# Kernel tuning notes

Measured on AMD Instinct MI355X. Metric: run time of the kernel, lower is better.

Reference implementation:

```python
import jax, jax.numpy as jnp
import numpy as np

B = 1024      # total windows (batch*windows_per_image)
W = 7         # window_size
T = W * W     # tokens per window = 49
C = 256       # scaled_emb_dim = emb_dim * 2**level
H = 8         # heads
D = C // H    # head_dim = 32
NUM_POS = 2 * W - 1


def _relative_pos():
    coords = np.arange(W)
    coords = np.stack(np.meshgrid(coords, coords, indexing='ij')).reshape(2, -1)
    rp = coords[:, :, None] - coords[:, None, :] + (W - 1)
    return jnp.asarray(rp, dtype=jnp.int32)  # (2, T, T)


def setup_inputs() -> dict:
    key = jax.random.key(0)
    ks = jax.random.split(key, 12)
    s = 0.02
    return {
        'x': jax.random.normal(ks[0], (B, T, C), dtype=jnp.float32),
        'relative_pos': _relative_pos(),
        'bias_table': jax.random.truncated_normal(ks[1], -2.0, 2.0, (H, NUM_POS, NUM_POS), dtype=jnp.float32) * s,
        'wq': jax.random.normal(ks[2], (C, H, D), dtype=jnp.float32) / np.sqrt(C),
        'bq': jnp.zeros((H, D), dtype=jnp.float32),
        'wk': jax.random.normal(ks[3], (C, H, D), dtype=jnp.float32) / np.sqrt(C),
        'bk': jnp.zeros((H, D), dtype=jnp.float32),
        'wv': jax.random.normal(ks[4], (C, H, D), dtype=jnp.float32) / np.sqrt(C),
        'bv': jnp.zeros((H, D), dtype=jnp.float32),
        'wo': jax.random.normal(ks[5], (H, D, C), dtype=jnp.float32) / np.sqrt(C),
        'bo': jnp.zeros((C,), dtype=jnp.float32),
        'dw': jax.random.normal(ks[6], (C, C), dtype=jnp.float32) / np.sqrt(C),
        'db': jnp.zeros((C,), dtype=jnp.float32),
    }


def reference(x, relative_pos, bias_table, wq, bq, wk, bk, wv, bv, wo, bo, dw, db):
    # QKV projections (flax DenseGeneral with bias)
    q = jnp.einsum('btc,chd->bthd', x, wq) + bq  # (B,T,H,D)
    k = jnp.einsum('btc,chd->bthd', x, wk) + bk
    v = jnp.einsum('btc,chd->bthd', x, wv) + bv

    # gathered relative position bias: (H, T, T)
    bias = bias_table[:, relative_pos[0], relative_pos[1]]

    # attention logits with query scaling (flax dot_product_attention)
    q = q / jnp.sqrt(jnp.asarray(D, dtype=q.dtype))
    logits = jnp.einsum('bqhd,bkhd->bhqk', q, k) + bias[None]
    attn = jax.nn.softmax(logits, axis=-1)

    out = jnp.einsum('bhqk,bkhd->bqhd', attn, v)
    y = jnp.einsum('bqhd,hdc->bqc', out, wo) + bo  # attention out projection
    y = jnp.einsum('btc,cf->btf', y, dw) + db      # trailing Dense(scaled_emb_dim)
    return y
```

## Files before the change

### kernel.cpp

```cpp
#include <hip/hip_runtime.h>
#include <stdint.h>

#define T 49
#define CCH 256

typedef __bf16 bf16x8 __attribute__((ext_vector_type(8)));
typedef float f32x4 __attribute__((ext_vector_type(4)));

static __device__ __forceinline__ unsigned short f2bf(float f){
  __bf16 h = (__bf16)f;
  return __builtin_bit_cast(unsigned short, h);
}
static __device__ __forceinline__ float bf2f(unsigned short h){
  return __builtin_bit_cast(float, ((uint32_t)h) << 16);
}
static __device__ __forceinline__ uint32_t pk2(float a, float b){
  return (uint32_t)f2bf(a) | ((uint32_t)f2bf(b) << 16);
}
static __device__ __forceinline__ f32x4 mfma16(bf16x8 a, bf16x8 b, f32x4 c){
  return __builtin_amdgcn_mfma_f32_16x16x32_bf16(a, b, c, 0, 0, 0);
}
#define SWZ(row) ((((row) & 7) << 4))

static __device__ __forceinline__ bf16x8 build_frag(uint32_t lo_w0, uint32_t lo_w1,
                                                    uint32_t hi_w0, uint32_t hi_w1,
                                                    int srcA, int srcB, bool use_hi){
  uint32_t a0 = (uint32_t)__shfl((int)lo_w0, srcA, 64);
  uint32_t c0 = (uint32_t)__shfl((int)hi_w0, srcA, 64);
  uint32_t a1 = (uint32_t)__shfl((int)lo_w1, srcA, 64);
  uint32_t c1 = (uint32_t)__shfl((int)hi_w1, srcA, 64);
  uint32_t a2 = (uint32_t)__shfl((int)lo_w0, srcB, 64);
  uint32_t c2 = (uint32_t)__shfl((int)hi_w0, srcB, 64);
  uint32_t a3 = (uint32_t)__shfl((int)lo_w1, srcB, 64);
  uint32_t c3 = (uint32_t)__shfl((int)hi_w1, srcB, 64);
  uint4 u = use_hi ? make_uint4(c0, c1, c2, c3) : make_uint4(a0, a1, a2, a3);
  return __builtin_bit_cast(bf16x8, u);
}


__global__ void prep_wqkvT(const float* __restrict__ wq, const float* __restrict__ wk,
                           const float* __restrict__ wv, unsigned short* __restrict__ out){
  int bk = blockIdx.x;
  int p = bk >> 8, kk = bk & 255;
  int n = threadIdx.x;
  const float* w = (p == 0) ? wq : (p == 1 ? wk : wv);
  float scl = (p == 0) ? 0.17677669529663687f : 1.0f;
  out[(size_t)(p * 256 + n) * 256 + kk] = f2bf(w[kk * 256 + n] * scl);
}

__global__ void prep_wodT(const float* __restrict__ wo, const float* __restrict__ dw,
                          unsigned short* __restrict__ out){
  int hd = blockIdx.x;
  int c = threadIdx.x;
  float s = 0.f;
  for (int cp = 0; cp < 256; ++cp) s = fmaf(wo[hd * 256 + cp], dw[cp * 256 + c], s);
  out[(size_t)c * 256 + hd] = f2bf(s);
}

__global__ void prep_misc(const int* __restrict__ rp, const float* __restrict__ btab,
                          const float* __restrict__ bq, const float* __restrict__ bk,
                          const float* __restrict__ bv, const float* __restrict__ bo,
                          const float* __restrict__ dwm, const float* __restrict__ db,
                          unsigned short* __restrict__ biasP, float* __restrict__ bqkv,
                          float* __restrict__ bod){
  int t = threadIdx.x;
  if (blockIdx.x == 0){
    for (int idx = t; idx < 768; idx += 256){
      int p = idx >> 8, n = idx & 255;
      float v = (p == 0) ? bq[n] * 0.17677669529663687f : (p == 1 ? bk[n] : bv[n]);
      bqkv[idx] = v;
    }
    float s = db[t];
    for (int cp = 0; cp < 256; ++cp) s = fmaf(bo[cp], dwm[cp * 256 + t], s);
    bod[t] = s;
  } else {
    int h = blockIdx.x - 1;
    for (int idx = t; idx < 4096; idx += 256){
      int r  = idx & 3;
      int lo = (idx >> 2) & 15;
      int g  = (idx >> 6) & 3;
      int nt = (idx >> 8) & 3;
      int jt = idx >> 10;
      int j = 16 * jt + 4 * g + r;
      int i = 16 * nt + lo;
      float v;
      if (j >= T) v = -1e30f;
      else if (i >= T) v = 0.f;
      else {
        int r0 = rp[i * 49 + j];
        int r1 = rp[2401 + i * 49 + j];
        v = btab[h * 169 + r0 * 13 + r1];
      }
      biasP[h * 4096 + idx] = f2bf(v);
    }
  }
}

__launch_bounds__(512, 6)
__global__ void qkv_kernel(const float* __restrict__ x,
                           const unsigned short* __restrict__ wqkvT,
                           const float* __restrict__ bqkv,
                           unsigned short* __restrict__ qg,
                           unsigned short* __restrict__ kg,
                           unsigned short* __restrict__ vtg){
  __shared__ unsigned short xs[64 * 256];

  const int b    = blockIdx.x;
  const int tid  = threadIdx.x;
  const int h    = tid >> 6;
  const int lane = tid & 63;
  const int g    = lane >> 4;
  const int lo   = lane & 15;
  char* xs_c = (char*)xs;
  const size_t bh = (size_t)(b * 8 + h);

  const float* xb = x + (size_t)b * T * CCH;
  {
    float4 vv[8];
    #pragma unroll
    for (int k2 = 0; k2 < 8; ++k2){
      int idx = tid + k2 * 512;
      int row = idx >> 6, c4 = idx & 63;
      vv[k2] = make_float4(0.f, 0.f, 0.f, 0.f);
      if (row < T) vv[k2] = reinterpret_cast<const float4*>(xb)[row * 64 + c4];
    }
    #pragma unroll
    for (int k2 = 0; k2 < 8; ++k2){
      int idx = tid + k2 * 512;
      int row = idx >> 6, c4 = idx & 63;
      *reinterpret_cast<uint2*>(xs_c + row * 512 + ((c4 * 8) ^ SWZ(row)))
          = make_uint2(pk2(vv[k2].x, vv[k2].y), pk2(vv[k2].z, vv[k2].w));
    }
  }
  __syncthreads();

  {
    f32x4 avc[4][2];
    #pragma unroll
    for (int mt = 0; mt < 4; ++mt)
      #pragma unroll
      for (int nt = 0; nt < 2; ++nt) avc[mt][nt] = f32x4{0,0,0,0};

    #pragma unroll 1
    for (int kb = 0; kb < 2; ++kb){
      bf16x8 wv[2][4];
      #pragma unroll
      for (int nt = 0; nt < 2; ++nt)
        #pragma unroll
        for (int q4 = 0; q4 < 4; ++q4)
          wv[nt][q4] = *reinterpret_cast<const bf16x8*>(
              wqkvT + (size_t)(512 + h * 32 + 16 * nt + lo) * 256 + (kb * 4 + q4) * 32 + 8 * g);
      #pragma unroll
      for (int q4 = 0; q4 < 4; ++q4){
        int kt = kb * 4 + q4;
        bf16x8 ax[4];
        #pragma unroll
        for (int mt = 0; mt < 4; ++mt){
          int row = 16 * mt + lo;
          ax[mt] = *reinterpret_cast<const bf16x8*>(xs_c + row * 512 + ((kt * 64 + 16 * g) ^ SWZ(row)));
        }
        #pragma unroll
        for (int nt = 0; nt < 2; ++nt)
          #pragma unroll
          for (int mt = 0; mt < 4; ++mt) avc[mt][nt] = mfma16(ax[mt], wv[nt][q4], avc[mt][nt]);
      }
    }
    #pragma unroll
    for (int nt = 0; nt < 2; ++nt){
      const float bvs = bqkv[512 + h * 32 + 16 * nt + lo];
      const int d = 16 * nt + lo;
      #pragma unroll
      for (int mt = 0; mt < 4; ++mt){
        f32x4 t = avc[mt][nt];
        *reinterpret_cast<uint2*>(vtg + (bh * 32 + d) * 64 + 16 * mt + 4 * g)
            = make_uint2(pk2(t[0] + bvs, t[1] + bvs), pk2(t[2] + bvs, t[3] + bvs));
      }
    }
  }

  {
    f32x4 akk[2][4];
    #pragma unroll
    for (int mt = 0; mt < 2; ++mt)
      #pragma unroll
      for (int nt = 0; nt < 4; ++nt) akk[mt][nt] = f32x4{0,0,0,0};

    #pragma unroll 1
    for (int kb = 0; kb < 2; ++kb){
      bf16x8 wk[2][4];
      #pragma unroll
      for (int mt = 0; mt < 2; ++mt)
        #pragma unroll
        for (int q4 = 0; q4 < 4; ++q4)
          wk[mt][q4] = *reinterpret_cast<const bf16x8*>(
              wqkvT + (size_t)(256 + h * 32 + 16 * mt + lo) * 256 + (kb * 4 + q4) * 32 + 8 * g);
      #pragma unroll
      for (int q4 = 0; q4 < 4; ++q4){
        int kt = kb * 4 + q4;
        bf16x8 bx[4];
        #pragma unroll
        for (int nt = 0; nt < 4; ++nt){
          int row = 16 * nt + lo;
          bx[nt] = *reinterpret_cast<const bf16x8*>(xs_c + row * 512 + ((kt * 64 + 16 * g) ^ SWZ(row)));
        }
        #pragma unroll
        for (int mt = 0; mt < 2; ++mt)
          #pragma unroll
          for (int nt = 0; nt < 4; ++nt) akk[mt][nt] = mfma16(wk[mt][q4], bx[nt], akk[mt][nt]);
      }
    }
    #pragma unroll
    for (int mt = 0; mt < 2; ++mt){
      const float4 b4 = *reinterpret_cast<const float4*>(bqkv + 256 + h * 32 + 16 * mt + 4 * g);
      #pragma unroll
      for (int nt = 0; nt < 4; ++nt){
        f32x4 t = akk[mt][nt];
        t[0] += b4.x; t[1] += b4.y; t[2] += b4.z; t[3] += b4.w;
        *reinterpret_cast<uint2*>(kg + (bh * 64 + 16 * nt + lo) * 32 + 16 * mt + 4 * g)
            = make_uint2(pk2(t[0], t[1]), pk2(t[2], t[3]));
      }
    }
  }

  {
    f32x4 aq[2][4];
    #pragma unroll
    for (int mt = 0; mt < 2; ++mt)
      #pragma unroll
      for (int nt = 0; nt < 4; ++nt) aq[mt][nt] = f32x4{0,0,0,0};

    #pragma unroll 1
    for (int kb = 0; kb < 2; ++kb){
      bf16x8 wq2[2][4];
      #pragma unroll
      for (int mt = 0; mt < 2; ++mt)
        #pragma unroll
        for (int q4 = 0; q4 < 4; ++q4)
          wq2[mt][q4] = *reinterpret_cast<const bf16x8*>(
              wqkvT + (size_t)(h * 32 + 16 * mt + lo) * 256 + (kb * 4 + q4) * 32 + 8 * g);
      #pragma unroll
      for (int q4 = 0; q4 < 4; ++q4){
        int kt = kb * 4 + q4;
        bf16x8 bx[4];
        #pragma unroll
        for (int nt = 0; nt < 4; ++nt){
          int row = 16 * nt + lo;
          bx[nt] = *reinterpret_cast<const bf16x8*>(xs_c + row * 512 + ((kt * 64 + 16 * g) ^ SWZ(row)));
        }
        #pragma unroll
        for (int mt = 0; mt < 2; ++mt)
          #pragma unroll
          for (int nt = 0; nt < 4; ++nt) aq[mt][nt] = mfma16(wq2[mt][q4], bx[nt], aq[mt][nt]);
      }
    }
    #pragma unroll
    for (int mt = 0; mt < 2; ++mt){
      const float4 b4 = *reinterpret_cast<const float4*>(bqkv + h * 32 + 16 * mt + 4 * g);
      #pragma unroll
      for (int nt = 0; nt < 4; ++nt){
        f32x4 t = aq[mt][nt];
        t[0] += b4.x; t[1] += b4.y; t[2] += b4.z; t[3] += b4.w;
        *reinterpret_cast<uint2*>(qg + (bh * 64 + 16 * nt + lo) * 32 + 16 * mt + 4 * g)
            = make_uint2(pk2(t[0], t[1]), pk2(t[2], t[3]));
      }
    }
  }
}

__launch_bounds__(512, 4)
__global__ void attn_out_kernel(const unsigned short* __restrict__ qg,
                                const unsigned short* __restrict__ kg,
                                const unsigned short* __restrict__ vtg,
                                const unsigned short* __restrict__ biasP,
                                const unsigned short* __restrict__ wodT,
                                const float* __restrict__ bod,
                                float* __restrict__ y){
  __shared__ unsigned short outs[64 * 256];

  const int b    = blockIdx.x;
  const int tid  = threadIdx.x;
  const int h    = tid >> 6;
  const int lane = tid & 63;
  const int g    = lane >> 4;
  const int lo   = lane & 15;
  char* os_c = (char*)outs;
  const size_t bh = (size_t)(b * 8 + h);

  const int  srcA = lo + 16 * ((2 * g) & 3);
  const int  srcB = lo + 16 * ((2 * g + 1) & 3);
  const bool ghi  = (g >= 2);

  bf16x8 ak[4], fq[4], av[2][2];
  #pragma unroll
  for (int jt = 0; jt < 4; ++jt)
    ak[jt] = *reinterpret_cast<const bf16x8*>(kg + (bh * 64 + 16 * jt + lo) * 32 + 8 * g);
  #pragma unroll
  for (int nt = 0; nt < 4; ++nt)
    fq[nt] = *reinterpret_cast<const bf16x8*>(qg + (bh * 64 + 16 * nt + lo) * 32 + 8 * g);
  #pragma unroll
  for (int dt = 0; dt < 2; ++dt)
    #pragma unroll
    for (int ktj = 0; ktj < 2; ++ktj)
      av[dt][ktj] = *reinterpret_cast<const bf16x8*>(
          vtg + (bh * 32 + 16 * dt + lo) * 64 + 32 * ktj + 8 * g);

  #pragma unroll 1
  for (int nt = 0; nt < 4; ++nt){
    uint2 bb[4];
    #pragma unroll
    for (int jt = 0; jt < 4; ++jt)
      bb[jt] = *reinterpret_cast<const uint2*>(
          biasP + h * 4096 + jt * 1024 + nt * 256 + (g * 16 + lo) * 4);
    f32x4 lacc[4];
    #pragma unroll
    for (int jt = 0; jt < 4; ++jt){
      lacc[jt] = mfma16(ak[jt], fq[nt], f32x4{0,0,0,0});
      lacc[jt][0] += bf2f((unsigned short)(bb[jt].x & 0xffff));
      lacc[jt][1] += bf2f((unsigned short)(bb[jt].x >> 16));
      lacc[jt][2] += bf2f((unsigned short)(bb[jt].y & 0xffff));
      lacc[jt][3] += bf2f((unsigned short)(bb[jt].y >> 16));
    }
    float m = -3.0e38f;
    #pragma unroll
    for (int jt = 0; jt < 4; ++jt)
      #pragma unroll
      for (int r = 0; r < 4; ++r) m = fmaxf(m, lacc[jt][r]);
    m = fmaxf(m, __shfl_xor(m, 16, 64));
    m = fmaxf(m, __shfl_xor(m, 32, 64));
    float ssum = 0.f;
    uint32_t pw[4][2];
    #pragma unroll
    for (int jt = 0; jt < 4; ++jt){
      f32x4 t = lacc[jt];
      #pragma unroll
      for (int r = 0; r < 4; ++r){
        t[r] = exp2f((t[r] - m) * 1.4426950408889634f);
        ssum += t[r];
      }
      pw[jt][0] = pk2(t[0], t[1]);
      pw[jt][1] = pk2(t[2], t[3]);
    }
    ssum += __shfl_xor(ssum, 16, 64);
    ssum += __shfl_xor(ssum, 32, 64);
    const float r0 = 1.f / ssum;

    bf16x8 pf0 = build_frag(pw[0][0], pw[0][1], pw[1][0], pw[1][1], srcA, srcB, ghi);
    bf16x8 pf1 = build_frag(pw[2][0], pw[2][1], pw[3][0], pw[3][1], srcA, srcB, ghi);

    const int i = 16 * nt + lo;
    #pragma unroll
    for (int dt = 0; dt < 2; ++dt){
      f32x4 oacc = mfma16(av[dt][0], pf0, f32x4{0,0,0,0});
      oacc = mfma16(av[dt][1], pf1, oacc);
      *reinterpret_cast<uint2*>(os_c + i * 512 + ((h * 64 + dt * 32 + g * 8) ^ SWZ(i)))
          = make_uint2(pk2(oacc[0] * r0, oacc[1] * r0), pk2(oacc[2] * r0, oacc[3] * r0));
    }
  }
  __syncthreads();

  f32x4 facc[4][2];
  #pragma unroll
  for (int mt = 0; mt < 4; ++mt)
    #pragma unroll
    for (int nt = 0; nt < 2; ++nt) facc[mt][nt] = f32x4{0,0,0,0};

  #pragma unroll 1
  for (int kb = 0; kb < 2; ++kb){
    bf16x8 wod[2][4];
    #pragma unroll
    for (int nt = 0; nt < 2; ++nt)
      #pragma unroll
      for (int q4 = 0; q4 < 4; ++q4)
        wod[nt][q4] = *reinterpret_cast<const bf16x8*>(
            wodT + (size_t)(h * 32 + nt * 16 + lo) * 256 + (kb * 4 + q4) * 32 + 8 * g);
    #pragma unroll
    for (int q4 = 0; q4 < 4; ++q4){
      int kt = kb * 4 + q4;
      bf16x8 a[4];
      #pragma unroll
      for (int mt = 0; mt < 4; ++mt){
        int row = 16 * mt + lo;
        a[mt] = *reinterpret_cast<const bf16x8*>(os_c + row * 512 + ((kt * 64 + 16 * g) ^ SWZ(row)));
      }
      #pragma unroll
      for (int nt = 0; nt < 2; ++nt)
        #pragma unroll
        for (int mt = 0; mt < 4; ++mt) facc[mt][nt] = mfma16(a[mt], wod[nt][q4], facc[mt][nt]);
    }
  }
  #pragma unroll
  for (int nt = 0; nt < 2; ++nt){
    int c = h * 32 + nt * 16 + lo;
    float bd = bod[c];
    #pragma unroll
    for (int mt = 0; mt < 4; ++mt)
      #pragma unroll
      for (int r = 0; r < 4; ++r){
        int i = 16 * mt + 4 * g + r;
        if (i < T) y[((size_t)b * T + i) * CCH + c] = facc[mt][nt][r] + bd;
      }
  }
}

__launch_bounds__(512, 4)
__global__ void wmsa_mono(const float* __restrict__ x,
                          const unsigned short* __restrict__ wqkvT,
                          const unsigned short* __restrict__ wodT,
                          const unsigned short* __restrict__ biasP,
                          const float* __restrict__ bqkv,
                          const float* __restrict__ bod,
                          float* __restrict__ y){
  __shared__ unsigned short xs[64 * 256];
  __shared__ unsigned short vts[8 * 32 * 64];

  const int b    = blockIdx.x;
  const int tid  = threadIdx.x;
  const int h    = tid >> 6;
  const int lane = tid & 63;
  const int g    = lane >> 4;
  const int lo   = lane & 15;
  char* xs_c = (char*)xs;

  const float* xb = x + (size_t)b * T * CCH;
  {
    float4 vv[8];
    #pragma unroll
    for (int k2 = 0; k2 < 8; ++k2){
      int idx = tid + k2 * 512;
      int row = idx >> 6, c4 = idx & 63;
      vv[k2] = make_float4(0.f, 0.f, 0.f, 0.f);
      if (row < T) vv[k2] = reinterpret_cast<const float4*>(xb)[row * 64 + c4];
    }
    #pragma unroll
    for (int k2 = 0; k2 < 8; ++k2){
      int idx = tid + k2 * 512;
      int row = idx >> 6, c4 = idx & 63;
      *reinterpret_cast<uint2*>(xs_c + row * 512 + ((c4 * 8) ^ SWZ(row)))
          = make_uint2(pk2(vv[k2].x, vv[k2].y), pk2(vv[k2].z, vv[k2].w));
    }
  }
  __syncthreads();

  const int  srcA = lo + 16 * ((2 * g) & 3);
  const int  srcB = lo + 16 * ((2 * g + 1) & 3);
  const bool ghi  = (g >= 2);

  {
    f32x4 avc[4][2];
    #pragma unroll
    for (int mt = 0; mt < 4; ++mt)
      #pragma unroll
      for (int nt = 0; nt < 2; ++nt) avc[mt][nt] = f32x4{0,0,0,0};
    #pragma unroll 1
    for (int kb = 0; kb < 2; ++kb){
      bf16x8 wv[2][4];
      #pragma unroll
      for (int nt = 0; nt < 2; ++nt)
        #pragma unroll
        for (int q4 = 0; q4 < 4; ++q4)
          wv[nt][q4] = *reinterpret_cast<const bf16x8*>(
              wqkvT + (size_t)(512 + h * 32 + 16 * nt + lo) * 256 + (kb * 4 + q4) * 32 + 8 * g);
      #pragma unroll
      for (int q4 = 0; q4 < 4; ++q4){
        int kt = kb * 4 + q4;
        bf16x8 ax[4];
        #pragma unroll
        for (int mt = 0; mt < 4; ++mt){
          int row = 16 * mt + lo;
          ax[mt] = *reinterpret_cast<const bf16x8*>(xs_c + row * 512 + ((kt * 64 + 16 * g) ^ SWZ(row)));
        }
        #pragma unroll
        for (int nt = 0; nt < 2; ++nt)
          #pragma unroll
          for (int mt = 0; mt < 4; ++mt) avc[mt][nt] = mfma16(ax[mt], wv[nt][q4], avc[mt][nt]);
      }
    }
    #pragma unroll
    for (int nt = 0; nt < 2; ++nt){
      const float bvs = bqkv[512 + h * 32 + 16 * nt + lo];
      const int d = 16 * nt + lo;
      #pragma unroll
      for (int mt = 0; mt < 4; ++mt){
        f32x4 t = avc[mt][nt];
        *reinterpret_cast<uint2*>((char*)vts + h * 4096 + d * 128 + ((mt * 32 + g * 8) ^ SWZ(d)))
            = make_uint2(pk2(t[0] + bvs, t[1] + bvs), pk2(t[2] + bvs, t[3] + bvs));
      }
    }
  }

  bf16x8 fk[4], fq[4];
  {
    f32x4 aq[2][4], akk[2][4];
    #pragma unroll
    for (int mt = 0; mt < 2; ++mt)
      #pragma unroll
      for (int nt = 0; nt < 4; ++nt){ aq[mt][nt] = f32x4{0,0,0,0}; akk[mt][nt] = f32x4{0,0,0,0}; }
    #pragma unroll 1
    for (int kb = 0; kb < 4; ++kb){
      bf16x8 wq2[2][2], wk2[2][2];
      #pragma unroll
      for (int mt = 0; mt < 2; ++mt)
        #pragma unroll
        for (int q2 = 0; q2 < 2; ++q2){
          wq2[mt][q2] = *reinterpret_cast<const bf16x8*>(
              wqkvT + (size_t)(h * 32 + 16 * mt + lo) * 256 + (kb * 2 + q2) * 32 + 8 * g);
          wk2[mt][q2] = *reinterpret_cast<const bf16x8*>(
              wqkvT + (size_t)(256 + h * 32 + 16 * mt + lo) * 256 + (kb * 2 + q2) * 32 + 8 * g);
        }
      #pragma unroll
      for (int q2 = 0; q2 < 2; ++q2){
        int kt = kb * 2 + q2;
        bf16x8 bx[4];
        #pragma unroll
        for (int nt = 0; nt < 4; ++nt){
          int row = 16 * nt + lo;
          bx[nt] = *reinterpret_cast<const bf16x8*>(xs_c + row * 512 + ((kt * 64 + 16 * g) ^ SWZ(row)));
        }
        #pragma unroll
        for (int mt = 0; mt < 2; ++mt)
          #pragma unroll
          for (int nt = 0; nt < 4; ++nt){
            aq[mt][nt]  = mfma16(wq2[mt][q2], bx[nt], aq[mt][nt]);
            akk[mt][nt] = mfma16(wk2[mt][q2], bx[nt], akk[mt][nt]);
          }
      }
    }
    uint32_t pq[2][4][2], pkk[2][4][2];
    #pragma unroll
    for (int mt = 0; mt < 2; ++mt){
      const float4 b4q = *reinterpret_cast<const float4*>(bqkv + h * 32 + 16 * mt + 4 * g);
      const float4 b4k = *reinterpret_cast<const float4*>(bqkv + 256 + h * 32 + 16 * mt + 4 * g);
      #pragma unroll
      for (int nt = 0; nt < 4; ++nt){
        f32x4 tq = aq[mt][nt], tk = akk[mt][nt];
        tq[0] += b4q.x; tq[1] += b4q.y; tq[2] += b4q.z; tq[3] += b4q.w;
        tk[0] += b4k.x; tk[1] += b4k.y; tk[2] += b4k.z; tk[3] += b4k.w;
        pq[mt][nt][0]  = pk2(tq[0], tq[1]); pq[mt][nt][1]  = pk2(tq[2], tq[3]);
        pkk[mt][nt][0] = pk2(tk[0], tk[1]); pkk[mt][nt][1] = pk2(tk[2], tk[3]);
      }
    }
    #pragma unroll
    for (int nt = 0; nt < 4; ++nt){
      fq[nt] = build_frag(pq[0][nt][0],  pq[0][nt][1],  pq[1][nt][0],  pq[1][nt][1],  srcA, srcB, ghi);
      fk[nt] = build_frag(pkk[0][nt][0], pkk[0][nt][1], pkk[1][nt][0], pkk[1][nt][1], srcA, srcB, ghi);
    }
  }
  __syncthreads();

  const char* vb = (const char*)vts + h * 4096;
  #pragma unroll 1
  for (int nt = 0; nt < 4; ++nt){
    uint2 bb[4];
    #pragma unroll
    for (int jt = 0; jt < 4; ++jt)
      bb[jt] = *reinterpret_cast<const uint2*>(
          biasP + h * 4096 + jt * 1024 + nt * 256 + (g * 16 + lo) * 4);
    f32x4 lacc[4];
    #pragma unroll
    for (int jt = 0; jt < 4; ++jt){
      lacc[jt] = mfma16(fk[jt], fq[nt], f32x4{0,0,0,0});
      lacc[jt][0] += bf2f((unsigned short)(bb[jt].x & 0xffff));
      lacc[jt][1] += bf2f((unsigned short)(bb[jt].x >> 16));
      lacc[jt][2] += bf2f((unsigned short)(bb[jt].y & 0xffff));
      lacc[jt][3] += bf2f((unsigned short)(bb[jt].y >> 16));
    }
    float m = -3.0e38f;
    #pragma unroll
    for (int jt = 0; jt < 4; ++jt)
      #pragma unroll
      for (int r = 0; r < 4; ++r) m = fmaxf(m, lacc[jt][r]);
    m = fmaxf(m, __shfl_xor(m, 16, 64));
    m = fmaxf(m, __shfl_xor(m, 32, 64));
    float ssum = 0.f;
    uint32_t pw[4][2];
    #pragma unroll
    for (int jt = 0; jt < 4; ++jt){
      f32x4 t = lacc[jt];
      #pragma unroll
      for (int r = 0; r < 4; ++r){
        t[r] = exp2f((t[r] - m) * 1.4426950408889634f);
        ssum += t[r];
      }
      pw[jt][0] = pk2(t[0], t[1]);
      pw[jt][1] = pk2(t[2], t[3]);
    }
    ssum += __shfl_xor(ssum, 16, 64);
    ssum += __shfl_xor(ssum, 32, 64);
    const float r0 = 1.f / ssum;
    bf16x8 pf0 = build_frag(pw[0][0], pw[0][1], pw[1][0], pw[1][1], srcA, srcB, ghi);
    bf16x8 pf1 = build_frag(pw[2][0], pw[2][1], pw[3][0], pw[3][1], srcA, srcB, ghi);
    const int i = 16 * nt + lo;
    #pragma unroll
    for (int dt = 0; dt < 2; ++dt){
      int row = 16 * dt + lo;
      bf16x8 av0 = *reinterpret_cast<const bf16x8*>(vb + row * 128 + ((16 * g) ^ SWZ(row)));
      bf16x8 av1 = *reinterpret_cast<const bf16x8*>(vb + row * 128 + ((64 + 16 * g) ^ SWZ(row)));
      f32x4 oacc = mfma16(av0, pf0, f32x4{0,0,0,0});
      oacc = mfma16(av1, pf1, oacc);
      *reinterpret_cast<uint2*>(xs_c + i * 512 + ((h * 64 + dt * 32 + g * 8) ^ SWZ(i)))
          = make_uint2(pk2(oacc[0] * r0, oacc[1] * r0), pk2(oacc[2] * r0, oacc[3] * r0));
    }
  }
  __syncthreads();

  f32x4 facc[4][2];
  #pragma unroll
  for (int mt = 0; mt < 4; ++mt)
    #pragma unroll
    for (int nt = 0; nt < 2; ++nt) facc[mt][nt] = f32x4{0,0,0,0};
  #pragma unroll 1
  for (int kb = 0; kb < 2; ++kb){
    bf16x8 wod[2][4];
    #pragma unroll
    for (int nt = 0; nt < 2; ++nt)
      #pragma unroll
      for (int q4 = 0; q4 < 4; ++q4)
        wod[nt][q4] = *reinterpret_cast<const bf16x8*>(
            wodT + (size_t)(h * 32 + nt * 16 + lo) * 256 + (kb * 4 + q4) * 32 + 8 * g);
    #pragma unroll
    for (int q4 = 0; q4 < 4; ++q4){
      int kt = kb * 4 + q4;
      bf16x8 a[4];
      #pragma unroll
      for (int mt = 0; mt < 4; ++mt){
        int row = 16 * mt + lo;
        a[mt] = *reinterpret_cast<const bf16x8*>(xs_c + row * 512 + ((kt * 64 + 16 * g) ^ SWZ(row)));
      }
      #pragma unroll
      for (int nt = 0; nt < 2; ++nt)
        #pragma unroll
        for (int mt = 0; mt < 4; ++mt) facc[mt][nt] = mfma16(a[mt], wod[nt][q4], facc[mt][nt]);
    }
  }
  #pragma unroll
  for (int nt = 0; nt < 2; ++nt){
    int c = h * 32 + nt * 16 + lo;
    float bd = bod[c];
    #pragma unroll
    for (int mt = 0; mt < 4; ++mt)
      #pragma unroll
      for (int r = 0; r < 4; ++r){
        int i = 16 * mt + 4 * g + r;
        if (i < T) y[((size_t)b * T + i) * CCH + c] = facc[mt][nt][r] + bd;
      }
  }
}

extern "C" void kernel_launch(void* const* d_in, const int* in_sizes, int n_in,
                              void* d_out, int out_size, void* d_ws, size_t ws_size,
                              hipStream_t stream){
  const float* x    = (const float*)d_in[0];
  const int*   rp   = (const int*)d_in[1];
  const float* btab = (const float*)d_in[2];
  const float* wq   = (const float*)d_in[3];
  const float* bq   = (const float*)d_in[4];
  const float* wk   = (const float*)d_in[5];
  const float* bk   = (const float*)d_in[6];
  const float* wv   = (const float*)d_in[7];
  const float* bv   = (const float*)d_in[8];
  const float* wo   = (const float*)d_in[9];
  const float* bo   = (const float*)d_in[10];
  const float* dw   = (const float*)d_in[11];
  const float* db   = (const float*)d_in[12];
  float* y = (float*)d_out;

  char* ws = (char*)d_ws;
  const size_t QKV_BYTES = 33554432ull;
  const size_t BIG_NEED  = 3 * QKV_BYTES + 393216 + 131072 + 65536 + 3072 + 1024;

  if (ws_size >= BIG_NEED){
    unsigned short* qg  = (unsigned short*)(ws);
    unsigned short* kg  = (unsigned short*)(ws + QKV_BYTES);
    unsigned short* vtg = (unsigned short*)(ws + 2 * QKV_BYTES);
    char* wsp = ws + 3 * QKV_BYTES;
    unsigned short* wqkvT = (unsigned short*)(wsp);
    unsigned short* wodT  = (unsigned short*)(wsp + 393216);
    unsigned short* biasP = (unsigned short*)(wsp + 524288);
    float* bqkv           = (float*)(wsp + 589824);
    float* bod            = (float*)(wsp + 592896);

    prep_wqkvT<<<768, 256, 0, stream>>>(wq, wk, wv, wqkvT);
    prep_wodT<<<256, 256, 0, stream>>>(wo, dw, wodT);
    prep_misc<<<9, 256, 0, stream>>>(rp, btab, bq, bk, bv, bo, dw, db, biasP, bqkv, bod);
    qkv_kernel<<<1024, 512, 0, stream>>>(x, wqkvT, bqkv, qg, kg, vtg);
    attn_out_kernel<<<1024, 512, 0, stream>>>(qg, kg, vtg, biasP, wodT, bod, y);
  } else {
    unsigned short* wqkvT = (unsigned short*)(ws);
    unsigned short* wodT  = (unsigned short*)(ws + 393216);
    unsigned short* biasP = (unsigned short*)(ws + 524288);
    float* bqkv           = (float*)(ws + 589824);
    float* bod            = (float*)(ws + 592896);

    prep_wqkvT<<<768, 256, 0, stream>>>(wq, wk, wv, wqkvT);
    prep_wodT<<<256, 256, 0, stream>>>(wo, dw, wodT);
    prep_misc<<<9, 256, 0, stream>>>(rp, btab, bq, bk, bv, bo, dw, db, biasP, bqkv, bod);
    wmsa_mono<<<1024, 512, 0, stream>>>(x, wqkvT, wodT, biasP, bqkv, bod, y);
  }
}
```

Before: 160.7 us.

## Split attention and output projection into separate kernels; process two windows per QKV block

The QKV kernel now stages two windows per block, so each weight fragment loaded from global memory is reused across 128 rows instead of 64. Attention becomes a standalone kernel with one wave per (window, head) that writes bf16 outputs to a new workspace buffer. A dense token-tiled GEMM kernel then applies the fused output projection over 64-token tiles without the 49→64 padding waste. The cost is an extra global round trip for the attention output, one more launch, and a larger workspace requirement.

Result: slower. 165.4 us (+2.9%).

```diff
diff --git a/kernel.cpp b/kernel.cpp
--- a/kernel.cpp
+++ b/kernel.cpp
@@ -96,26 +96,26 @@
   }
 }
 
-__launch_bounds__(512, 6)
-__global__ void qkv_kernel(const float* __restrict__ x,
-                           const unsigned short* __restrict__ wqkvT,
-                           const float* __restrict__ bqkv,
-                           unsigned short* __restrict__ qg,
-                           unsigned short* __restrict__ kg,
-                           unsigned short* __restrict__ vtg){
-  __shared__ unsigned short xs[64 * 256];
-
-  const int b    = blockIdx.x;
+__launch_bounds__(512, 4)
+__global__ void qkv2_kernel(const float* __restrict__ x,
+                            const unsigned short* __restrict__ wqkvT,
+                            const float* __restrict__ bqkv,
+                            unsigned short* __restrict__ qg,
+                            unsigned short* __restrict__ kg,
+                            unsigned short* __restrict__ vtg){
+  __shared__ unsigned short xs[128 * 256];
+
+  const int b2   = blockIdx.x;
   const int tid  = threadIdx.x;
   const int h    = tid >> 6;
   const int lane = tid & 63;
   const int g    = lane >> 4;
   const int lo   = lane & 15;
   char* xs_c = (char*)xs;
-  const size_t bh = (size_t)(b * 8 + h);
-
-  const float* xb = x + (size_t)b * T * CCH;
-  {
+
+  #pragma unroll 1
+  for (int half = 0; half < 2; ++half){
+    const float* xb = x + (size_t)(2 * b2 + half) * T * CCH;
     float4 vv[8];
     #pragma unroll
     for (int k2 = 0; k2 < 8; ++k2){
@@ -128,18 +128,21 @@
     for (int k2 = 0; k2 < 8; ++k2){
       int idx = tid + k2 * 512;
       int row = idx >> 6, c4 = idx & 63;
-      *reinterpret_cast<uint2*>(xs_c + row * 512 + ((c4 * 8) ^ SWZ(row)))
+      int drow = half * 64 + row;
+      *reinterpret_cast<uint2*>(xs_c + drow * 512 + ((c4 * 8) ^ SWZ(drow)))
           = make_uint2(pk2(vv[k2].x, vv[k2].y), pk2(vv[k2].z, vv[k2].w));
     }
   }
   __syncthreads();
 
   {
-    f32x4 avc[4][2];
-    #pragma unroll
-    for (int mt = 0; mt < 4; ++mt)
-      #pragma unroll
-      for (int nt = 0; nt < 2; ++nt) avc[mt][nt] = f32x4{0,0,0,0};
+    f32x4 avc[2][4][2];
+    #pragma unroll
+    for (int w2 = 0; w2 < 2; ++w2)
+      #pragma unroll
+      for (int mt = 0; mt < 4; ++mt)
+        #pragma unroll
+        for (int nt = 0; nt < 2; ++nt) avc[w2][mt][nt] = f32x4{0,0,0,0};
 
     #pragma unroll 1
     for (int kb = 0; kb < 2; ++kb){
@@ -153,37 +156,47 @@
       #pragma unroll
       for (int q4 = 0; q4 < 4; ++q4){
         int kt = kb * 4 + q4;
-        bf16x8 ax[4];
+        #pragma unroll
+        for (int w2 = 0; w2 < 2; ++w2){
+          bf16x8 ax[4];
+          #pragma unroll
+          for (int mt = 0; mt < 4; ++mt){
+            int row = w2 * 64 + 16 * mt + lo;
+            ax[mt] = *reinterpret_cast<const bf16x8*>(xs_c + row * 512 + ((kt * 64 + 16 * g) ^ SWZ(row)));
+          }
+          #pragma unroll
+          for (int nt = 0; nt < 2; ++nt)
+            #pragma unroll
+            for (int mt = 0; mt < 4; ++mt)
+              avc[w2][mt][nt] = mfma16(ax[mt], wv[nt][q4], avc[w2][mt][nt]);
+        }
+      }
+    }
+    #pragma unroll
+    for (int w2 = 0; w2 < 2; ++w2){
+      const size_t bh = (size_t)((2 * b2 + w2) * 8 + h);
+      #pragma unroll
+      for (int nt = 0; nt < 2; ++nt){
+        const float bvs = bqkv[512 + h * 32 + 16 * nt + lo];
+        const int d = 16 * nt + lo;
         #pragma unroll
         for (int mt = 0; mt < 4; ++mt){
-          int row = 16 * mt + lo;
-          ax[mt] = *reinterpret_cast<const bf16x8*>(xs_c + row * 512 + ((kt * 64 + 16 * g) ^ SWZ(row)));
-        }
-        #pragma unroll
-        for (int nt = 0; nt < 2; ++nt)
-          #pragma unroll
-          for (int mt = 0; mt < 4; ++mt) avc[mt][nt] = mfma16(ax[mt], wv[nt][q4], avc[mt][nt]);
-      }
-    }
-    #pragma unroll
-    for (int nt = 0; nt < 2; ++nt){
-      const float bvs = bqkv[512 + h * 32 + 16 * nt + lo];
-      const int d = 16 * nt + lo;
-      #pragma unroll
-      for (int mt = 0; mt < 4; ++mt){
-        f32x4 t = avc[mt][nt];
-        *reinterpret_cast<uint2*>(vtg + (bh * 32 + d) * 64 + 16 * mt + 4 * g)
-            = make_uint2(pk2(t[0] + bvs, t[1] + bvs), pk2(t[2] + bvs, t[3] + bvs));
+          f32x4 t = avc[w2][mt][nt];
+          *reinterpret_cast<uint2*>(vtg + (bh * 32 + d) * 64 + 16 * mt + 4 * g)
+              = make_uint2(pk2(t[0] + bvs, t[1] + bvs), pk2(t[2] + bvs, t[3] + bvs));
+        }
       }
     }
   }
 
   {
-    f32x4 akk[2][4];
-    #pragma unroll
-    for (int mt = 0; mt < 2; ++mt)
-      #pragma unroll
-      for (int nt = 0; nt < 4; ++nt) akk[mt][nt] = f32x4{0,0,0,0};
+    f32x4 akk[2][2][4];
+    #pragma unroll
+    for (int w2 = 0; w2 < 2; ++w2)
+      #pragma unroll
+      for (int mt = 0; mt < 2; ++mt)
+        #pragma unroll
+        for (int nt = 0; nt < 4; ++nt) akk[w2][mt][nt] = f32x4{0,0,0,0};
 
     #pragma unroll 1
     for (int kb = 0; kb < 2; ++kb){
@@ -197,37 +210,47 @@
       #pragma unroll
       for (int q4 = 0; q4 < 4; ++q4){
         int kt = kb * 4 + q4;
-        bf16x8 bx[4];
+        #pragma unroll
+        for (int w2 = 0; w2 < 2; ++w2){
+          bf16x8 bx[4];
+          #pragma unroll
+          for (int nt = 0; nt < 4; ++nt){
+            int row = w2 * 64 + 16 * nt + lo;
+            bx[nt] = *reinterpret_cast<const bf16x8*>(xs_c + row * 512 + ((kt * 64 + 16 * g) ^ SWZ(row)));
+          }
+          #pragma unroll
+          for (int mt = 0; mt < 2; ++mt)
+            #pragma unroll
+            for (int nt = 0; nt < 4; ++nt)
+              akk[w2][mt][nt] = mfma16(wk[mt][q4], bx[nt], akk[w2][mt][nt]);
+        }
+      }
+    }
+    #pragma unroll
+    for (int w2 = 0; w2 < 2; ++w2){
+      const size_t bh = (size_t)((2 * b2 + w2) * 8 + h);
+      #pragma unroll
+      for (int mt = 0; mt < 2; ++mt){
+        const float4 b4 = *reinterpret_cast<const float4*>(bqkv + 256 + h * 32 + 16 * mt + 4 * g);
         #pragma unroll
         for (int nt = 0; nt < 4; ++nt){
-          int row = 16 * nt + lo;
-          bx[nt] = *reinterpret_cast<const bf16x8*>(xs_c + row * 512 + ((kt * 64 + 16 * g) ^ SWZ(row)));
-        }
-        #pragma unroll
-        for (int mt = 0; mt < 2; ++mt)
-          #pragma unroll
-          for (int nt = 0; nt < 4; ++nt) akk[mt][nt] = mfma16(wk[mt][q4], bx[nt], akk[mt][nt]);
-      }
-    }
-    #pragma unroll
-    for (int mt = 0; mt < 2; ++mt){
-      const float4 b4 = *reinterpret_cast<const float4*>(bqkv + 256 + h * 32 + 16 * mt + 4 * g);
-      #pragma unroll
-      for (int nt = 0; nt < 4; ++nt){
-        f32x4 t = akk[mt][nt];
-        t[0] += b4.x; t[1] += b4.y; t[2] += b4.z; t[3] += b4.w;
-        *reinterpret_cast<uint2*>(kg + (bh * 64 + 16 * nt + lo) * 32 + 16 * mt + 4 * g)
-            = make_uint2(pk2(t[0], t[1]), pk2(t[2], t[3]));
+          f32x4 t = akk[w2][mt][nt];
+          t[0] += b4.x; t[1] += b4.y; t[2] += b4.z; t[3] += b4.w;
+          *reinterpret_cast<uint2*>(kg + (bh * 64 + 16 * nt + lo) * 32 + 16 * mt + 4 * g)
+              = make_uint2(pk2(t[0], t[1]), pk2(t[2], t[3]));
+        }
       }
     }
   }
 
   {
-    f32x4 aq[2][4];
-    #pragma unroll
-    for (int mt = 0; mt < 2; ++mt)
-      #pragma unroll
-      for (int nt = 0; nt < 4; ++nt) aq[mt][nt] = f32x4{0,0,0,0};
+    f32x4 aq[2][2][4];
+    #pragma unroll
+    for (int w2 = 0; w2 < 2; ++w2)
+      #pragma unroll
+      for (int mt = 0; mt < 2; ++mt)
+        #pragma unroll
+        for (int nt = 0; nt < 4; ++nt) aq[w2][mt][nt] = f32x4{0,0,0,0};
 
     #pragma unroll 1
     for (int kb = 0; kb < 2; ++kb){
@@ -241,50 +264,55 @@
       #pragma unroll
       for (int q4 = 0; q4 < 4; ++q4){
         int kt = kb * 4 + q4;
-        bf16x8 bx[4];
+        #pragma unroll
+        for (int w2 = 0; w2 < 2; ++w2){
+          bf16x8 bx[4];
+          #pragma unroll
+          for (int nt = 0; nt < 4; ++nt){
+            int row = w2 * 64 + 16 * nt + lo;
+            bx[nt] = *reinterpret_cast<const bf16x8*>(xs_c + row * 512 + ((kt * 64 + 16 * g) ^ SWZ(row)));
+          }
+          #pragma unroll
+          for (int mt = 0; mt < 2; ++mt)
+            #pragma unroll
+            for (int nt = 0; nt < 4; ++nt)
+              aq[w2][mt][nt] = mfma16(wq2[mt][q4], bx[nt], aq[w2][mt][nt]);
+        }
+      }
+    }
+    #pragma unroll
+    for (int w2 = 0; w2 < 2; ++w2){
+      const size_t bh = (size_t)((2 * b2 + w2) * 8 + h);
+      #pragma unroll
+      for (int mt = 0; mt < 2; ++mt){
+        const float4 b4 = *reinterpret_cast<const float4*>(bqkv + h * 32 + 16 * mt + 4 * g);
         #pragma unroll
         for (int nt = 0; nt < 4; ++nt){
-          int row = 16 * nt + lo;
-          bx[nt] = *reinterpret_cast<const bf16x8*>(xs_c + row * 512 + ((kt * 64 + 16 * g) ^ SWZ(row)));
-        }
-        #pragma unroll
-        for (int mt = 0; mt < 2; ++mt)
-          #pragma unroll
-          for (int nt = 0; nt < 4; ++nt) aq[mt][nt] = mfma16(wq2[mt][q4], bx[nt], aq[mt][nt]);
-      }
-    }
-    #pragma unroll
-    for (int mt = 0; mt < 2; ++mt){
-      const float4 b4 = *reinterpret_cast<const float4*>(bqkv + h * 32 + 16 * mt + 4 * g);
-      #pragma unroll
-      for (int nt = 0; nt < 4; ++nt){
-        f32x4 t = aq[mt][nt];
-        t[0] += b4.x; t[1] += b4.y; t[2] += b4.z; t[3] += b4.w;
-        *reinterpret_cast<uint2*>(qg + (bh * 64 + 16 * nt + lo) * 32 + 16 * mt + 4 * g)
-            = make_uint2(pk2(t[0], t[1]), pk2(t[2], t[3]));
-      }
-    }
-  }
-}
-
-__launch_bounds__(512, 4)
-__global__ void attn_out_kernel(const unsigned short* __restrict__ qg,
-                                const unsigned short* __restrict__ kg,
-                                const unsigned short* __restrict__ vtg,
-                                const unsigned short* __restrict__ biasP,
-                                const unsigned short* __restrict__ wodT,
-                                const float* __restrict__ bod,
-                                float* __restrict__ y){
-  __shared__ unsigned short outs[64 * 256];
-
-  const int b    = blockIdx.x;
+          f32x4 t = aq[w2][mt][nt];
+          t[0] += b4.x; t[1] += b4.y; t[2] += b4.z; t[3] += b4.w;
+          *reinterpret_cast<uint2*>(qg + (bh * 64 + 16 * nt + lo) * 32 + 16 * mt + 4 * g)
+              = make_uint2(pk2(t[0], t[1]), pk2(t[2], t[3]));
+        }
+      }
+    }
+  }
+}
+
+__launch_bounds__(256, 4)
+__global__ void attn_b(const unsigned short* __restrict__ qg,
+                       const unsigned short* __restrict__ kg,
+                       const unsigned short* __restrict__ vtg,
+                       const unsigned short* __restrict__ biasP,
+                       unsigned short* __restrict__ og){
   const int tid  = threadIdx.x;
-  const int h    = tid >> 6;
+  const int wv_  = tid >> 6;
   const int lane = tid & 63;
   const int g    = lane >> 4;
   const int lo   = lane & 15;
-  char* os_c = (char*)outs;
-  const size_t bh = (size_t)(b * 8 + h);
+  const int task = blockIdx.x * 4 + wv_;
+  const int b    = task >> 3;
+  const int h    = task & 7;
+  const size_t bh = (size_t)task;
 
   const int  srcA = lo + 16 * ((2 * g) & 3);
   const int  srcB = lo + 16 * ((2 * g + 1) & 3);
@@ -320,11 +348,11 @@
       lacc[jt][2] += bf2f((unsigned short)(bb[jt].y & 0xffff));
       lacc[jt][3] += bf2f((unsigned short)(bb[jt].y >> 16));
     }
-    float m = -3.0e38f;
-    #pragma unroll
-    for (int jt = 0; jt < 4; ++jt)
-      #pragma unroll
-      for (int r = 0; r < 4; ++r) m = fmaxf(m, lacc[jt][r]);
+    float m01a = fmaxf(fmaxf(lacc[0][0], lacc[0][1]), fmaxf(lacc[0][2], lacc[0][3]));
+    float m01b = fmaxf(fmaxf(lacc[1][0], lacc[1][1]), fmaxf(lacc[1][2], lacc[1][3]));
+    float m23a = fmaxf(fmaxf(lacc[2][0], lacc[2][1]), fmaxf(lacc[2][2], lacc[2][3]));
+    float m23b = fmaxf(fmaxf(lacc[3][0], lacc[3][1]), fmaxf(lacc[3][2], lacc[3][3]));
+    float m = fmaxf(fmaxf(m01a, m01b), fmaxf(m23a, m23b));
     m = fmaxf(m, __shfl_xor(m, 16, 64));
     m = fmaxf(m, __shfl_xor(m, 32, 64));
     float ssum = 0.f;
@@ -352,53 +380,62 @@
     for (int dt = 0; dt < 2; ++dt){
       f32x4 oacc = mfma16(av[dt][0], pf0, f32x4{0,0,0,0});
       oacc = mfma16(av[dt][1], pf1, oacc);
-      *reinterpret_cast<uint2*>(os_c + i * 512 + ((h * 64 + dt * 32 + g * 8) ^ SWZ(i)))
-          = make_uint2(pk2(oacc[0] * r0, oacc[1] * r0), pk2(oacc[2] * r0, oacc[3] * r0));
-    }
-  }
-  __syncthreads();
-
-  f32x4 facc[4][2];
+      if (i < T)
+        *reinterpret_cast<uint2*>(og + ((size_t)b * T + i) * 256 + h * 32 + 16 * dt + 4 * g)
+            = make_uint2(pk2(oacc[0] * r0, oacc[1] * r0), pk2(oacc[2] * r0, oacc[3] * r0));
+    }
+  }
+}
+
+__launch_bounds__(512, 4)
+__global__ void out_c(const unsigned short* __restrict__ og,
+                      const unsigned short* __restrict__ wodT,
+                      const float* __restrict__ bod,
+                      float* __restrict__ y){
+  const int tid  = threadIdx.x;
+  const int w    = tid >> 6;
+  const int lane = tid & 63;
+  const int g    = lane >> 4;
+  const int lo   = lane & 15;
+  const int tok0 = blockIdx.x * 64;
+
+  f32x4 acc[2][4];
   #pragma unroll
-  for (int mt = 0; mt < 4; ++mt)
-    #pragma unroll
-    for (int nt = 0; nt < 2; ++nt) facc[mt][nt] = f32x4{0,0,0,0};
-
-  #pragma unroll 1
-  for (int kb = 0; kb < 2; ++kb){
-    bf16x8 wod[2][4];
-    #pragma unroll
-    for (int nt = 0; nt < 2; ++nt)
-      #pragma unroll
-      for (int q4 = 0; q4 < 4; ++q4)
-        wod[nt][q4] = *reinterpret_cast<const bf16x8*>(
-            wodT + (size_t)(h * 32 + nt * 16 + lo) * 256 + (kb * 4 + q4) * 32 + 8 * g);
-    #pragma unroll
-    for (int q4 = 0; q4 < 4; ++q4){
-      int kt = kb * 4 + q4;
-      bf16x8 a[4];
-      #pragma unroll
-      for (int mt = 0; mt < 4; ++mt){
-        int row = 16 * mt + lo;
-        a[mt] = *reinterpret_cast<const bf16x8*>(os_c + row * 512 + ((kt * 64 + 16 * g) ^ SWZ(row)));
-      }
-      #pragma unroll
-      for (int nt = 0; nt < 2; ++nt)
-        #pragma unroll
-        for (int mt = 0; mt < 4; ++mt) facc[mt][nt] = mfma16(a[mt], wod[nt][q4], facc[mt][nt]);
-    }
-  }
+  for (int mt = 0; mt < 2; ++mt)
+    #pragma unroll
+    for (int nt = 0; nt < 4; ++nt) acc[mt][nt] = f32x4{0,0,0,0};
+
+  #pragma unroll 2
+  for (int kt = 0; kt < 8; ++kt){
+    bf16x8 aw[2], bo_[4];
+    #pragma unroll
+    for (int mt = 0; mt < 2; ++mt)
+      aw[mt] = *reinterpret_cast<const bf16x8*>(
+          wodT + (size_t)(32 * w + 16 * mt + lo) * 256 + kt * 32 + 8 * g);
+    #pragma unroll
+    for (int nt = 0; nt < 4; ++nt)
+      bo_[nt] = *reinterpret_cast<const bf16x8*>(
+          og + (size_t)(tok0 + 16 * nt + lo) * 256 + kt * 32 + 8 * g);
+    #pragma unroll
+    for (int mt = 0; mt < 2; ++mt)
+      #pragma unroll
+      for (int nt = 0; nt < 4; ++nt) acc[mt][nt] = mfma16(aw[mt], bo_[nt], acc[mt][nt]);
+  }
+
   #pragma unroll
-  for (int nt = 0; nt < 2; ++nt){
-    int c = h * 32 + nt * 16 + lo;
-    float bd = bod[c];
-    #pragma unroll
-    for (int mt = 0; mt < 4; ++mt)
-      #pragma unroll
-      for (int r = 0; r < 4; ++r){
-        int i = 16 * mt + 4 * g + r;
-        if (i < T) y[((size_t)b * T + i) * CCH + c] = facc[mt][nt][r] + bd;
-      }
+  for (int mt = 0; mt < 2; ++mt){
+    const int cb = 32 * w + 16 * mt + 4 * g;
+    const float4 b4 = *reinterpret_cast<const float4*>(bod + cb);
+    #pragma unroll
+    for (int nt = 0; nt < 4; ++nt){
+      const int tok = tok0 + 16 * nt + lo;
+      float4 o;
+      o.x = acc[mt][nt][0] + b4.x;
+      o.y = acc[mt][nt][1] + b4.y;
+      o.z = acc[mt][nt][2] + b4.z;
+      o.w = acc[mt][nt][3] + b4.w;
+      *reinterpret_cast<float4*>(y + (size_t)tok * 256 + cb) = o;
+    }
   }
 }
 
@@ -666,13 +703,16 @@
 
   char* ws = (char*)d_ws;
   const size_t QKV_BYTES = 33554432ull;
-  const size_t BIG_NEED  = 3 * QKV_BYTES + 393216 + 131072 + 65536 + 3072 + 1024;
-
-  if (ws_size >= BIG_NEED){
+  const size_t OG_BYTES  = 25690112ull;
+  const size_t PREP      = 593920ull;
+  const size_t NEED3     = 3 * QKV_BYTES + OG_BYTES + PREP;
+
+  if (ws_size >= NEED3){
     unsigned short* qg  = (unsigned short*)(ws);
     unsigned short* kg  = (unsigned short*)(ws + QKV_BYTES);
     unsigned short* vtg = (unsigned short*)(ws + 2 * QKV_BYTES);
-    char* wsp = ws + 3 * QKV_BYTES;
+    unsigned short* og  = (unsigned short*)(ws + 3 * QKV_BYTES);
+    char* wsp = ws + 3 * QKV_BYTES + OG_BYTES;
     unsigned short* wqkvT = (unsigned short*)(wsp);
     unsigned short* wodT  = (unsigned short*)(wsp + 393216);
     unsigned short* biasP = (unsigned short*)(wsp + 524288);
@@ -682,8 +722,9 @@
     prep_wqkvT<<<768, 256, 0, stream>>>(wq, wk, wv, wqkvT);
     prep_wodT<<<256, 256, 0, stream>>>(wo, dw, wodT);
     prep_misc<<<9, 256, 0, stream>>>(rp, btab, bq, bk, bv, bo, dw, db, biasP, bqkv, bod);
-    qkv_kernel<<<1024, 512, 0, stream>>>(x, wqkvT, bqkv, qg, kg, vtg);
-    attn_out_kernel<<<1024, 512, 0, stream>>>(qg, kg, vtg, biasP, wodT, bod, y);
+    qkv2_kernel<<<512, 512, 0, stream>>>(x, wqkvT, bqkv, qg, kg, vtg);
+    attn_b<<<2048, 256, 0, stream>>>(qg, kg, vtg, biasP, og);
+    out_c<<<784, 512, 0, stream>>>(og, wodT, bod, y);
   } else {
     unsigned short* wqkvT = (unsigned short*)(ws);
     unsigned short* wodT  = (unsigned short*)(ws + 393216);
```
